# Optimization experiments

Measured on AMD Instinct MI355X. Metric: run time of the kernel, lower is better.

## Reference

```python
import jax, jax.numpy as jnp
import numpy as np

N_E = 8192
E_DIM = 256
BETA = 0.25
SIGMA = 0.1


def setup_inputs() -> dict:
    key = jax.random.key(0)
    kz, ke = jax.random.split(key)
    z = jax.random.normal(kz, (16, 256, 32, 32), dtype=jnp.float32)
    # torch init: uniform(-1/n_e, 1/n_e)
    emb = jax.random.uniform(ke, (N_E, E_DIM), minval=-1.0 / N_E, maxval=1.0 / N_E, dtype=jnp.float32)
    return {"z": z, "emb": emb}


def _vq_forward(z, emb, beta=BETA, sigma=SIGMA):
    b, c, h, w = z.shape  # c == e_dim
    z_bhwc = jnp.transpose(z, (0, 2, 3, 1))  # b h w c
    zf = z_bhwc.reshape(-1, c)  # [b*h*w, c]

    # d[i, n] = ||zf_i||^2 + ||e_n||^2 - 2 zf_i . e_n
    e2 = jnp.sum(emb ** 2, axis=1)  # [n_e]
    d = jnp.sum(zf ** 2, axis=1, keepdims=True) + e2 - 2.0 * (zf @ emb.T)  # [bhw, n_e]

    # codebook-codebook pairwise distances
    d1 = e2[:, None] + e2[None, :] - 2.0 * (emb @ emb.T)  # [n_e, n_e]
    # torch.kthvalue(d1, 2, 0): 2nd smallest along dim 0, per column
    min_dist = jnp.sort(d1, axis=0)[1]  # [n_e]
    total_min_distance = jnp.sum(min_dist)
    codebookvariance = jnp.std(min_dist, ddof=1)  # torch.std is unbiased

    min_encoding_indices = jnp.argmin(d, axis=1)  # [bhw]
    # d[range, argmin] == row-wise min
    distances = jnp.min(d, axis=1).reshape(b, h, w)
    # rbf: exp(-(d^2).mean(axis=1) / (2*sigma^2)) -> [b, w]
    distances = jnp.exp(-jnp.mean(distances ** 2, axis=1) / (2.0 * sigma ** 2))

    z_q = jnp.take(emb, min_encoding_indices, axis=0).reshape(b, h, w, c)

    sg = jax.lax.stop_gradient
    # legacy=True branch
    loss = (jnp.mean((sg(z_q) - z_bhwc) ** 2)
            + beta * jnp.mean((z_q - sg(z_bhwc)) ** 2)
            - total_min_distance)

    # straight-through estimator
    z_q = z_bhwc + sg(z_q - z_bhwc)
    z_q_bchw = jnp.transpose(z_q, (0, 3, 1, 2))  # b c h w (contiguous)
    # torch .view(b, h*w, e_dim) on contiguous bchw buffer: raw reshape
    z_flattened1 = z_q_bchw.reshape(b, h * w, c)

    return (z_q_bchw, loss, distances, min_encoding_indices,
            z_flattened1, codebookvariance, total_min_distance)


def reference(z, emb):
    return _vq_forward(z, emb)
```

## Files before the change

kernel.cpp:

```cpp
#include <hip/hip_runtime.h>
#include <stdint.h>

#define N_E   8192
#define EDIM  256
#define NB    16
#define HH    32
#define WW    32
#define HW    1024
#define NI    16384
#define NELEM 4194304

#define MARGIN_D1 1e-9f

#define O_ZQ   0
#define O_LOSS 4194304
#define O_DIST 4194305
#define O_IDX  4194817
#define O_ZFL  4211201
#define O_CBV  8405505
#define O_TMD  8405506

#define WS_IDX   0x0
#define WS_DMIN  0x20000
#define WS_E2    0x40000
#define WS_Z2    0x50000
#define WS_MSE   0x60000
#define WS_MIND  0x61000
#define WS_PZ    0x70000
#define WS_PD1   0x270000
#define WS_ZAH   0x400000
#define WS_ZAL   0xC00000
#define WS_EBH   0x1400000
#define WS_EBL   0x1800000

typedef __attribute__((ext_vector_type(8))) short bf16x8;
typedef __attribute__((ext_vector_type(4))) float f32x4;

__device__ __forceinline__ short f2bf(float f) {
    unsigned u = __float_as_uint(f);
    u += 0x7fffu + ((u >> 16) & 1u);
    return (short)(u >> 16);
}
__device__ __forceinline__ float bf2f(short h) {
    return __uint_as_float(((unsigned)(unsigned short)h) << 16);
}
__device__ __forceinline__ unsigned keyf(float f) {
    unsigned b = __float_as_uint(f);
    return (b & 0x80000000u) ? ~b : (b | 0x80000000u);
}
__device__ __forceinline__ float unkeyf(unsigned k) {
    return (k & 0x80000000u) ? __uint_as_float(k ^ 0x80000000u) : __uint_as_float(~k);
}
__device__ __forceinline__ void ins2(unsigned long long& a1, unsigned long long& a2,
                                     unsigned long long v) {
    if (v < a1) { a2 = a1; a1 = v; } else if (v < a2) { a2 = v; }
}
__device__ __forceinline__ void mrg2(unsigned long long& a1, unsigned long long& a2,
                                     unsigned long long b1, unsigned long long b2) {
    unsigned long long n1 = a1 < b1 ? a1 : b1;
    unsigned long long mx = a1 < b1 ? b1 : a1;
    unsigned long long mn = a2 < b2 ? a2 : b2;
    a1 = n1; a2 = mx < mn ? mx : mn;
}

__global__ void k_init(double* __restrict__ mse) {
    if (threadIdx.x == 0) *mse = 0.0;
}

__global__ void k_e2(const float* __restrict__ emb, float* __restrict__ e2) {
    int row  = blockIdx.x * 4 + (threadIdx.x >> 6);
    int lane = threadIdx.x & 63;
    float4 v = *reinterpret_cast<const float4*>(emb + (size_t)row * EDIM + lane * 4);
    float s = v.x * v.x + v.y * v.y + v.z * v.z + v.w * v.w;
    #pragma unroll
    for (int m = 32; m; m >>= 1) s += __shfl_xor(s, m);
    if (lane == 0) e2[row] = s;
}

__global__ void k_z2(const float* __restrict__ z, float* __restrict__ z2) {
    int i = blockIdx.x * 256 + threadIdx.x;
    int b = i >> 10, hw = i & 1023;
    const float* p = z + (size_t)b * EDIM * HW + hw;
    float s = 0.f;
    #pragma unroll 8
    for (int c = 0; c < EDIM; ++c) { float v = p[(size_t)c * HW]; s += v * v; }
    z2[i] = s;
}

__global__ void k_convert_z(const float* __restrict__ z,
                            bf16x8* __restrict__ zAh, bf16x8* __restrict__ zAl) {
    __shared__ float lds[64][65];
    const int t   = threadIdx.x;
    const int hw0 = blockIdx.x * 64;
    const int c0  = blockIdx.y * 64;
    const int b   = blockIdx.z;
    #pragma unroll
    for (int cc = 0; cc < 4; ++cc) {
        const int cl = cc * 16 + (t >> 4);
        const float4 v = *reinterpret_cast<const float4*>(
            z + ((size_t)(b * 256 + c0 + cl) << 10) + hw0 + (t & 15) * 4);
        lds[cl][(t & 15) * 4 + 0] = v.x; lds[cl][(t & 15) * 4 + 1] = v.y;
        lds[cl][(t & 15) * 4 + 2] = v.z; lds[cl][(t & 15) * 4 + 3] = v.w;
    }
    __syncthreads();
    const int hl = t & 63;
    const int i  = b * 1024 + hw0 + hl;
    const int ig = i >> 4, r = i & 15;
    #pragma unroll
    for (int half = 0; half < 2; ++half) {
        const int kqi = (t >> 6) + half * 4;
        const int kq  = (c0 >> 3) + kqi;
        bf16x8 oh, ol;
        #pragma unroll
        for (int j = 0; j < 8; ++j) {
            const float f = lds[kqi * 8 + j][hl];
            const short h = f2bf(f);
            oh[j] = h;
            ol[j] = f2bf(f - bf2f(h));
        }
        zAh[(ig * 32 + kq) * 16 + r] = oh;
        zAl[(ig * 32 + kq) * 16 + r] = ol;
    }
}

__global__ void k_convert_e(const float* __restrict__ emb,
                            bf16x8* __restrict__ eBh, bf16x8* __restrict__ eBl) {
    const int t  = threadIdx.x;
    const int kq = t & 31;
    const int n  = blockIdx.x * 8 + (t >> 5);
    const float4 u = *reinterpret_cast<const float4*>(emb + (size_t)n * EDIM + kq * 8);
    const float4 v = *reinterpret_cast<const float4*>(emb + (size_t)n * EDIM + kq * 8 + 4);
    const float fv[8] = {u.x, u.y, u.z, u.w, v.x, v.y, v.z, v.w};
    bf16x8 oh, ol;
    #pragma unroll
    for (int j = 0; j < 8; ++j) {
        const short h = f2bf(fv[j]);
        oh[j] = h;
        ol[j] = f2bf(fv[j] - bf2f(h));
    }
    eBh[((n >> 4) * 32 + kq) * 16 + (n & 15)] = oh;
    eBl[((n >> 4) * 32 + kq) * 16 + (n & 15)] = ol;
}

__launch_bounds__(256, 2)
__global__ void k_cand(const bf16x8* __restrict__ zAh, const bf16x8* __restrict__ zAl,
                       const bf16x8* __restrict__ eBh, const bf16x8* __restrict__ eBl,
                       const float* __restrict__ z2, const float* __restrict__ e2,
                       unsigned long long* __restrict__ pz) {
    const int t = threadIdx.x;
    const int w = t >> 6, l = t & 63;
    const int lo16 = l & 15, hi4 = l >> 4;
    const int iblk = blockIdx.x, chunk = blockIdx.y;
    const int ig0 = (iblk * 128 + w * 32) >> 4;

    float z2r[2][4];
    #pragma unroll
    for (int ig = 0; ig < 2; ++ig)
        #pragma unroll
        for (int reg = 0; reg < 4; ++reg)
            z2r[ig][reg] = z2[iblk * 128 + w * 32 + ig * 16 + hi4 * 4 + reg];

    unsigned long long t1[2][4], t2[2][4];
    #pragma unroll
    for (int ig = 0; ig < 2; ++ig)
        #pragma unroll
        for (int reg = 0; reg < 4; ++reg) { t1[ig][reg] = ~0ull; t2[ig][reg] = ~0ull; }

    for (int ns = 0; ns < 8; ++ns) {
        const int n0 = chunk * 1024 + ns * 128;
        f32x4 acc[2][8];
        #pragma unroll
        for (int ig = 0; ig < 2; ++ig)
            #pragma unroll
            for (int cg = 0; cg < 8; ++cg) acc[ig][cg] = (f32x4){0.f, 0.f, 0.f, 0.f};

        #pragma unroll
        for (int st = 0; st < 8; ++st) {
            const bf16x8 ah0 = zAh[((ig0 + 0) * 32 + st * 4 + hi4) * 16 + lo16];
            const bf16x8 ah1 = zAh[((ig0 + 1) * 32 + st * 4 + hi4) * 16 + lo16];
            const bf16x8 al0 = zAl[((ig0 + 0) * 32 + st * 4 + hi4) * 16 + lo16];
            const bf16x8 al1 = zAl[((ig0 + 1) * 32 + st * 4 + hi4) * 16 + lo16];
            #pragma unroll
            for (int cg = 0; cg < 8; ++cg) {
                const bf16x8 bh = eBh[(((n0 >> 4) + cg) * 32 + st * 4 + hi4) * 16 + lo16];
                const bf16x8 bl = eBl[(((n0 >> 4) + cg) * 32 + st * 4 + hi4) * 16 + lo16];
                acc[0][cg] = __builtin_amdgcn_mfma_f32_16x16x32_bf16(ah0, bh, acc[0][cg], 0, 0, 0);
                acc[0][cg] = __builtin_amdgcn_mfma_f32_16x16x32_bf16(ah0, bl, acc[0][cg], 0, 0, 0);
                acc[0][cg] = __builtin_amdgcn_mfma_f32_16x16x32_bf16(al0, bh, acc[0][cg], 0, 0, 0);
                acc[1][cg] = __builtin_amdgcn_mfma_f32_16x16x32_bf16(ah1, bh, acc[1][cg], 0, 0, 0);
                acc[1][cg] = __builtin_amdgcn_mfma_f32_16x16x32_bf16(ah1, bl, acc[1][cg], 0, 0, 0);
                acc[1][cg] = __builtin_amdgcn_mfma_f32_16x16x32_bf16(al1, bh, acc[1][cg], 0, 0, 0);
            }
        }
        float e2v[8];
        #pragma unroll
        for (int cg = 0; cg < 8; ++cg) e2v[cg] = e2[n0 + cg * 16 + lo16];
        #pragma unroll
        for (int ig = 0; ig < 2; ++ig) {
            #pragma unroll
            for (int reg = 0; reg < 4; ++reg) {
                #pragma unroll
                for (int cg = 0; cg < 8; ++cg) {
                    const float d = fmaf(-2.f, acc[ig][cg][reg], z2r[ig][reg] + e2v[cg]);
                    const unsigned long long pk =
                        ((unsigned long long)keyf(d) << 32) | (unsigned)(n0 + cg * 16 + lo16);
                    ins2(t1[ig][reg], t2[ig][reg], pk);
                }
            }
        }
    }
    #pragma unroll
    for (int ig = 0; ig < 2; ++ig) {
        #pragma unroll
        for (int reg = 0; reg < 4; ++reg) {
            unsigned long long a1 = t1[ig][reg], a2 = t2[ig][reg];
            #pragma unroll
            for (int o = 1; o < 16; o <<= 1) {
                const unsigned long long b1 = __shfl_xor(a1, o);
                const unsigned long long b2 = __shfl_xor(a2, o);
                mrg2(a1, a2, b1, b2);
            }
            if (lo16 == 0) {
                const int row = iblk * 128 + w * 32 + ig * 16 + hi4 * 4 + reg;
                pz[(row * 8 + chunk) * 2 + 0] = a1;
                pz[(row * 8 + chunk) * 2 + 1] = a2;
            }
        }
    }
}

__launch_bounds__(256, 2)
__global__ void k_cand_d1(const bf16x8* __restrict__ eBh, const bf16x8* __restrict__ eBl,
                          const float* __restrict__ e2,
                          unsigned long long* __restrict__ pd1) {
    const int t = threadIdx.x;
    const int w = t >> 6, l = t & 63;
    const int lo16 = l & 15, hi4 = l >> 4;
    const int iblk = blockIdx.x, chunk = blockIdx.y;
    const int ig0 = (iblk * 128 + w * 32) >> 4;

    unsigned long long t1[2][4], t2[2][4];
    #pragma unroll
    for (int ig = 0; ig < 2; ++ig)
        #pragma unroll
        for (int reg = 0; reg < 4; ++reg) { t1[ig][reg] = ~0ull; t2[ig][reg] = ~0ull; }

    for (int ns = 0; ns < 8; ++ns) {
        const int n0 = chunk * 1024 + ns * 128;
        f32x4 acc[2][8];
        #pragma unroll
        for (int ig = 0; ig < 2; ++ig)
            #pragma unroll
            for (int cg = 0; cg < 8; ++cg) acc[ig][cg] = (f32x4){0.f, 0.f, 0.f, 0.f};

        #pragma unroll
        for (int st = 0; st < 8; ++st) {
            const bf16x8 ah0 = eBh[((ig0 + 0) * 32 + st * 4 + hi4) * 16 + lo16];
            const bf16x8 ah1 = eBh[((ig0 + 1) * 32 + st * 4 + hi4) * 16 + lo16];
            const bf16x8 al0 = eBl[((ig0 + 0) * 32 + st * 4 + hi4) * 16 + lo16];
            const bf16x8 al1 = eBl[((ig0 + 1) * 32 + st * 4 + hi4) * 16 + lo16];
            #pragma unroll
            for (int cg = 0; cg < 8; ++cg) {
                const bf16x8 bh = eBh[(((n0 >> 4) + cg) * 32 + st * 4 + hi4) * 16 + lo16];
                const bf16x8 bl = eBl[(((n0 >> 4) + cg) * 32 + st * 4 + hi4) * 16 + lo16];
                acc[0][cg] = __builtin_amdgcn_mfma_f32_16x16x32_bf16(ah0, bh, acc[0][cg], 0, 0, 0);
                acc[0][cg] = __builtin_amdgcn_mfma_f32_16x16x32_bf16(ah0, bl, acc[0][cg], 0, 0, 0);
                acc[0][cg] = __builtin_amdgcn_mfma_f32_16x16x32_bf16(al0, bh, acc[0][cg], 0, 0, 0);
                acc[1][cg] = __builtin_amdgcn_mfma_f32_16x16x32_bf16(ah1, bh, acc[1][cg], 0, 0, 0);
                acc[1][cg] = __builtin_amdgcn_mfma_f32_16x16x32_bf16(ah1, bl, acc[1][cg], 0, 0, 0);
                acc[1][cg] = __builtin_amdgcn_mfma_f32_16x16x32_bf16(al1, bh, acc[1][cg], 0, 0, 0);
            }
        }
        float e2v[8];
        #pragma unroll
        for (int cg = 0; cg < 8; ++cg) e2v[cg] = e2[n0 + cg * 16 + lo16];
        #pragma unroll
        for (int ig = 0; ig < 2; ++ig) {
            #pragma unroll
            for (int reg = 0; reg < 4; ++reg) {
                #pragma unroll
                for (int cg = 0; cg < 8; ++cg) {
                    const float q = fmaf(-2.f, acc[ig][cg][reg], e2v[cg]);
                    const unsigned long long pk =
                        ((unsigned long long)keyf(q) << 32) | (unsigned)(n0 + cg * 16 + lo16);
                    ins2(t1[ig][reg], t2[ig][reg], pk);
                }
            }
        }
    }
    #pragma unroll
    for (int ig = 0; ig < 2; ++ig) {
        #pragma unroll
        for (int reg = 0; reg < 4; ++reg) {
            unsigned long long a1 = t1[ig][reg], a2 = t2[ig][reg];
            #pragma unroll
            for (int o = 1; o < 16; o <<= 1) {
                const unsigned long long b1 = __shfl_xor(a1, o);
                const unsigned long long b2 = __shfl_xor(a2, o);
                mrg2(a1, a2, b1, b2);
            }
            if (lo16 == 0) {
                const int row = iblk * 128 + w * 32 + ig * 16 + hi4 * 4 + reg;
                pd1[(row * 8 + chunk) * 2 + 0] = a1;
                pd1[(row * 8 + chunk) * 2 + 1] = a2;
            }
        }
    }
}

__global__ void k_zmerge(const float* __restrict__ z, const float* __restrict__ emb,
                         const float* __restrict__ z2, const float* __restrict__ e2,
                         const unsigned long long* __restrict__ pz,
                         int* __restrict__ idxi, float* __restrict__ dmin,
                         float* __restrict__ out_idx) {
    const int t = threadIdx.x, l = t & 63;
    const int row = blockIdx.x * 64 + (t >> 6) * 16 + (l >> 2);
    const int cs = (l >> 1) & 1, hf = l & 1;
    unsigned long long a1 = ~0ull, a2 = ~0ull;
    #pragma unroll
    for (int k = 0; k < 4; ++k)
        ins2(a1, a2, pz[row * 16 + (l & 3) * 4 + k]);
    #pragma unroll
    for (int o = 1; o < 4; o <<= 1) {
        const unsigned long long b1 = __shfl_xor(a1, o);
        const unsigned long long b2 = __shfl_xor(a2, o);
        mrg2(a1, a2, b1, b2);
    }
    const int n = (unsigned)(cs ? a2 : a1);
    const float* zp = z + ((size_t)(row >> 10) << 18) + (row & 1023);
    const float* ep = emb + (size_t)n * EDIM;
    float acc = 0.f;
    #pragma unroll 8
    for (int c = 0; c < 128; ++c) {
        const int cc = hf * 128 + c;
        acc = fmaf(zp[(size_t)cc << 10], ep[cc], acc);
    }
    const float total = acc + __shfl_xor(acc, 1);
    const float d = fmaf(-2.f, total, z2[row] + e2[n]);
    unsigned long long pk = ((unsigned long long)__float_as_uint(d) << 32) | (unsigned)n;
    const unsigned long long op = __shfl_xor(pk, 2);
    if (op < pk) pk = op;
    if ((l & 3) == 0) {
        const int ni = (int)(pk & 0xFFFFFFFFull);
        idxi[row] = ni;
        dmin[row] = __uint_as_float((unsigned)(pk >> 32));
        out_idx[row] = (float)ni;
    }
}

__global__ void k_d1merge(const float* __restrict__ emb, const float* __restrict__ e2,
                          const unsigned long long* __restrict__ pd1,
                          float* __restrict__ mind) {
    const int n = blockIdx.x * 256 + threadIdx.x;
    unsigned long long w1 = ~0ull, w2 = ~0ull;
    unsigned long long ent[16];
    #pragma unroll
    for (int e = 0; e < 16; ++e) { ent[e] = pd1[n * 16 + e]; ins2(w1, w2, ent[e]); }
    const float thr = unkeyf((unsigned)(w2 >> 32)) + MARGIN_D1;
    const float e2n = e2[n];
    const float* np = emb + (size_t)n * EDIM;
    float b1 = 3.4e38f, b2 = 3.4e38f;
    #pragma unroll 1
    for (int e = 0; e < 16; ++e) {
        const float af = unkeyf((unsigned)(ent[e] >> 32));
        if (af > thr) continue;
        const int m = (unsigned)ent[e];
        const float* ep = emb + (size_t)m * EDIM;
        float acc = 0.f;
        #pragma unroll 8
        for (int c = 0; c < EDIM; ++c) acc = fmaf(ep[c], np[c], acc);
        const float dv = (e2[m] + e2n) - 2.0f * acc;
        if (dv < b1) { b2 = b1; b1 = dv; } else if (dv < b2) { b2 = dv; }
    }
    mind[n] = b2;
}

__global__ void k_epilogue(const float* __restrict__ z, const float* __restrict__ emb,
                           const int* __restrict__ idxi,
                           float* __restrict__ out_zq, float* __restrict__ out_zfl,
                           double* __restrict__ mse) {
    const int j4 = blockIdx.x * 256 + threadIdx.x;
    const int j  = j4 * 4;
    const int b  = j >> 18;
    const int c  = (j >> 10) & 255;
    const int hw = j & 1023;
    const int ib = (b << 10) + hw;
    const float4 zv = *reinterpret_cast<const float4*>(z + j);
    const float q0 = emb[(size_t)idxi[ib + 0] * EDIM + c];
    const float q1 = emb[(size_t)idxi[ib + 1] * EDIM + c];
    const float q2 = emb[(size_t)idxi[ib + 2] * EDIM + c];
    const float q3 = emb[(size_t)idxi[ib + 3] * EDIM + c];
    const float d0 = q0 - zv.x, d1 = q1 - zv.y, d2 = q2 - zv.z, d3 = q3 - zv.w;
    const float4 st = {zv.x + d0, zv.y + d1, zv.z + d2, zv.w + d3};
    *reinterpret_cast<float4*>(out_zq + j) = st;
    out_zfl[j + 0] = st.x; out_zfl[j + 1] = st.y; out_zfl[j + 2] = st.z; out_zfl[j + 3] = st.w;

    double s = (double)(d0 * d0) + (double)(d1 * d1) + (double)(d2 * d2) + (double)(d3 * d3);
    #pragma unroll
    for (int m = 32; m; m >>= 1) s += __shfl_down(s, m);
    __shared__ double part[4];
    if ((threadIdx.x & 63) == 0) part[threadIdx.x >> 6] = s;
    __syncthreads();
    if (threadIdx.x == 0) atomicAdd(mse, part[0] + part[1] + part[2] + part[3]);
}

__global__ void k_distances(const float* __restrict__ dmin, float* __restrict__ out_d) {
    int t = threadIdx.x;
    int b = t >> 5, w = t & 31;
    float s = 0.f;
    #pragma unroll
    for (int h = 0; h < HH; ++h) {
        float d = dmin[(b << 10) + (h << 5) + w];
        s += d * d;
    }
    float mean = s * (1.0f / 32.0f);
    out_d[t] = expf(-mean / 0.02f);
}

__global__ void k_finalize(const float* __restrict__ mind, const double* __restrict__ mse,
                           float* __restrict__ out) {
    const int t = threadIdx.x;
    double s = 0.0, ss = 0.0;
    for (int n = t; n < N_E; n += 256) {
        const double v = (double)mind[n];
        s += v; ss += v * v;
    }
    #pragma unroll
    for (int m = 32; m; m >>= 1) { s += __shfl_down(s, m); ss += __shfl_down(ss, m); }
    __shared__ double rs[4], rss[4];
    if ((t & 63) == 0) { rs[t >> 6] = s; rss[t >> 6] = ss; }
    __syncthreads();
    if (t == 0) {
        const double S  = rs[0] + rs[1] + rs[2] + rs[3];
        const double SS = rss[0] + rss[1] + rss[2] + rss[3];
        const float tmd = (float)S;
        double var = (SS - S * S / (double)N_E) / (double)(N_E - 1);
        if (var < 0.0) var = 0.0;
        const float cbv = (float)sqrt(var);
        const float m1  = (float)(*mse / (double)NELEM);
        const float lossf = m1 + 0.25f * m1 - tmd;
        out[O_LOSS] = lossf;
        out[O_CBV]  = cbv;
        out[O_TMD]  = tmd;
    }
}

extern "C" void kernel_launch(void* const* d_in, const int* in_sizes, int n_in,
                              void* d_out, int out_size, void* d_ws, size_t ws_size,
                              hipStream_t stream) {
    const float* z   = (const float*)d_in[0];
    const float* emb = (const float*)d_in[1];
    float* out = (float*)d_out;
    char*  ws  = (char*)d_ws;

    int*      idxi = (int*)    (ws + WS_IDX);
    float*    dmin = (float*)  (ws + WS_DMIN);
    float*    e2   = (float*)  (ws + WS_E2);
    float*    z2   = (float*)  (ws + WS_Z2);
    double*   mse  = (double*) (ws + WS_MSE);
    float*    mind = (float*)  (ws + WS_MIND);
    unsigned long long* pz  = (unsigned long long*)(ws + WS_PZ);
    unsigned long long* pd1 = (unsigned long long*)(ws + WS_PD1);
    bf16x8*   zAh  = (bf16x8*) (ws + WS_ZAH);
    bf16x8*   zAl  = (bf16x8*) (ws + WS_ZAL);
    bf16x8*   eBh  = (bf16x8*) (ws + WS_EBH);
    bf16x8*   eBl  = (bf16x8*) (ws + WS_EBL);

    k_init     <<<1,    64,  0, stream>>>(mse);
    k_e2       <<<2048, 256, 0, stream>>>(emb, e2);
    k_z2       <<<64,   256, 0, stream>>>(z, z2);
    k_convert_z<<<dim3(16, 4, 16), 256, 0, stream>>>(z, zAh, zAl);
    k_convert_e<<<1024, 256, 0, stream>>>(emb, eBh, eBl);
    k_cand     <<<dim3(128, 8), 256, 0, stream>>>(zAh, zAl, eBh, eBl, z2, e2, pz);
    k_cand_d1  <<<dim3(64, 8),  256, 0, stream>>>(eBh, eBl, e2, pd1);
    k_zmerge   <<<256,  256, 0, stream>>>(z, emb, z2, e2, pz, idxi, dmin, out + O_IDX);
    k_d1merge  <<<32,   256, 0, stream>>>(emb, e2, pd1, mind);
    k_epilogue <<<4096, 256, 0, stream>>>(z, emb, idxi, out + O_ZQ, out + O_ZFL, mse);
    k_distances<<<1,    512, 0, stream>>>(dmin, out + O_DIST);
    k_finalize <<<1,    256, 0, stream>>>(mind, mse, out);
}
```

Before: 1.279 ms.

## Emit per-subchunk top-2 candidates, raise occupancy, parallelize codebook merge per wave

The candidate GEMM kernels no longer carry running top-2 arrays across the column loop. Each 128-column sub-chunk now reduces and writes its own top-2, which frees registers so launch bounds can go to 3 waves-per-EU occupancy; the MFMA issue order is also regrouped into batches of 4 B tiles. The codebook-pair merge now uses one wave per row with shuffle reductions and parallel exact rechecks, replacing the 32-block one-thread-per-row loop. In exchange, the candidate buffers grow eightfold; they are placed in unused regions of the output buffer to save workspace, and the merge kernels must read more candidates.

```diff
diff --git a/kernel.cpp b/kernel.cpp
--- a/kernel.cpp
+++ b/kernel.cpp
@@ -26,12 +26,10 @@
 #define WS_Z2    0x50000
 #define WS_MSE   0x60000
 #define WS_MIND  0x61000
-#define WS_PZ    0x70000
-#define WS_PD1   0x270000
-#define WS_ZAH   0x400000
-#define WS_ZAL   0xC00000
-#define WS_EBH   0x1400000
-#define WS_EBL   0x1800000
+#define WS_ZAH   0x100000
+#define WS_ZAL   0x900000
+#define WS_EBH   0x1100000
+#define WS_EBL   0x1500000
 
 typedef __attribute__((ext_vector_type(8))) short bf16x8;
 typedef __attribute__((ext_vector_type(4))) float f32x4;
@@ -142,7 +140,7 @@
     eBl[((n >> 4) * 32 + kq) * 16 + (n & 15)] = ol;
 }
 
-__launch_bounds__(256, 2)
+__launch_bounds__(256, 3)
 __global__ void k_cand(const bf16x8* __restrict__ zAh, const bf16x8* __restrict__ zAl,
                        const bf16x8* __restrict__ eBh, const bf16x8* __restrict__ eBl,
                        const float* __restrict__ z2, const float* __restrict__ e2,
@@ -160,14 +158,9 @@
         for (int reg = 0; reg < 4; ++reg)
             z2r[ig][reg] = z2[iblk * 128 + w * 32 + ig * 16 + hi4 * 4 + reg];
 
-    unsigned long long t1[2][4], t2[2][4];
-    #pragma unroll
-    for (int ig = 0; ig < 2; ++ig)
-        #pragma unroll
-        for (int reg = 0; reg < 4; ++reg) { t1[ig][reg] = ~0ull; t2[ig][reg] = ~0ull; }
-
+    #pragma unroll 1
     for (int ns = 0; ns < 8; ++ns) {
-        const int n0 = chunk * 1024 + ns * 128;
+        const int gcol = chunk * 64 + ns * 8;
         f32x4 acc[2][8];
         #pragma unroll
         for (int ig = 0; ig < 2; ++ig)
@@ -176,60 +169,71 @@
 
         #pragma unroll
         for (int st = 0; st < 8; ++st) {
-            const bf16x8 ah0 = zAh[((ig0 + 0) * 32 + st * 4 + hi4) * 16 + lo16];
-            const bf16x8 ah1 = zAh[((ig0 + 1) * 32 + st * 4 + hi4) * 16 + lo16];
-            const bf16x8 al0 = zAl[((ig0 + 0) * 32 + st * 4 + hi4) * 16 + lo16];
-            const bf16x8 al1 = zAl[((ig0 + 1) * 32 + st * 4 + hi4) * 16 + lo16];
+            const int arow = st * 4 + hi4;
+            const bf16x8 ah0 = zAh[((ig0 + 0) * 32 + arow) * 16 + lo16];
+            const bf16x8 ah1 = zAh[((ig0 + 1) * 32 + arow) * 16 + lo16];
+            const bf16x8 al0 = zAl[((ig0 + 0) * 32 + arow) * 16 + lo16];
+            const bf16x8 al1 = zAl[((ig0 + 1) * 32 + arow) * 16 + lo16];
             #pragma unroll
-            for (int cg = 0; cg < 8; ++cg) {
-                const bf16x8 bh = eBh[(((n0 >> 4) + cg) * 32 + st * 4 + hi4) * 16 + lo16];
-                const bf16x8 bl = eBl[(((n0 >> 4) + cg) * 32 + st * 4 + hi4) * 16 + lo16];
-                acc[0][cg] = __builtin_amdgcn_mfma_f32_16x16x32_bf16(ah0, bh, acc[0][cg], 0, 0, 0);
-                acc[0][cg] = __builtin_amdgcn_mfma_f32_16x16x32_bf16(ah0, bl, acc[0][cg], 0, 0, 0);
-                acc[0][cg] = __builtin_amdgcn_mfma_f32_16x16x32_bf16(al0, bh, acc[0][cg], 0, 0, 0);
-                acc[1][cg] = __builtin_amdgcn_mfma_f32_16x16x32_bf16(ah1, bh, acc[1][cg], 0, 0, 0);
-                acc[1][cg] = __builtin_amdgcn_mfma_f32_16x16x32_bf16(ah1, bl, acc[1][cg], 0, 0, 0);
-                acc[1][cg] = __builtin_amdgcn_mfma_f32_16x16x32_bf16(al1, bh, acc[1][cg], 0, 0, 0);
+            for (int cgb = 0; cgb < 8; cgb += 4) {
+                bf16x8 bh[4], bl[4];
+                #pragma unroll
+                for (int q = 0; q < 4; ++q) {
+                    bh[q] = eBh[((gcol + cgb + q) * 32 + arow) * 16 + lo16];
+                    bl[q] = eBl[((gcol + cgb + q) * 32 + arow) * 16 + lo16];
+                }
+                #pragma unroll
+                for (int q = 0; q < 4; ++q)
+                    acc[0][cgb+q] = __builtin_amdgcn_mfma_f32_16x16x32_bf16(ah0, bh[q], acc[0][cgb+q], 0, 0, 0);
+                #pragma unroll
+                for (int q = 0; q < 4; ++q)
+                    acc[1][cgb+q] = __builtin_amdgcn_mfma_f32_16x16x32_bf16(ah1, bh[q], acc[1][cgb+q], 0, 0, 0);
+                #pragma unroll
+                for (int q = 0; q < 4; ++q)
+                    acc[0][cgb+q] = __builtin_amdgcn_mfma_f32_16x16x32_bf16(ah0, bl[q], acc[0][cgb+q], 0, 0, 0);
+                #pragma unroll
+                for (int q = 0; q < 4; ++q)
+                    acc[1][cgb+q] = __builtin_amdgcn_mfma_f32_16x16x32_bf16(ah1, bl[q], acc[1][cgb+q], 0, 0, 0);
+                #pragma unroll
+                for (int q = 0; q < 4; ++q)
+                    acc[0][cgb+q] = __builtin_amdgcn_mfma_f32_16x16x32_bf16(al0, bh[q], acc[0][cgb+q], 0, 0, 0);
+                #pragma unroll
+                for (int q = 0; q < 4; ++q)
+                    acc[1][cgb+q] = __builtin_amdgcn_mfma_f32_16x16x32_bf16(al1, bh[q], acc[1][cgb+q], 0, 0, 0);
             }
         }
         float e2v[8];
         #pragma unroll
-        for (int cg = 0; cg < 8; ++cg) e2v[cg] = e2[n0 + cg * 16 + lo16];
+        for (int cg = 0; cg < 8; ++cg) e2v[cg] = e2[(gcol + cg) * 16 + lo16];
         #pragma unroll
         for (int ig = 0; ig < 2; ++ig) {
             #pragma unroll
             for (int reg = 0; reg < 4; ++reg) {
+                unsigned long long t1 = ~0ull, t2 = ~0ull;
                 #pragma unroll
                 for (int cg = 0; cg < 8; ++cg) {
                     const float d = fmaf(-2.f, acc[ig][cg][reg], z2r[ig][reg] + e2v[cg]);
                     const unsigned long long pk =
-                        ((unsigned long long)keyf(d) << 32) | (unsigned)(n0 + cg * 16 + lo16);
-                    ins2(t1[ig][reg], t2[ig][reg], pk);
+                        ((unsigned long long)keyf(d) << 32) | (unsigned)((gcol + cg) * 16 + lo16);
+                    ins2(t1, t2, pk);
+                }
+                #pragma unroll
+                for (int o = 1; o < 16; o <<= 1) {
+                    const unsigned long long b1 = __shfl_xor(t1, o);
+                    const unsigned long long b2 = __shfl_xor(t2, o);
+                    mrg2(t1, t2, b1, b2);
+                }
+                if (lo16 == 0) {
+                    const int row = iblk * 128 + w * 32 + ig * 16 + hi4 * 4 + reg;
+                    pz[((size_t)row * 64 + chunk * 8 + ns) * 2 + 0] = t1;
+                    pz[((size_t)row * 64 + chunk * 8 + ns) * 2 + 1] = t2;
                 }
             }
         }
     }
-    #pragma unroll
-    for (int ig = 0; ig < 2; ++ig) {
-        #pragma unroll
-        for (int reg = 0; reg < 4; ++reg) {
-            unsigned long long a1 = t1[ig][reg], a2 = t2[ig][reg];
-            #pragma unroll
-            for (int o = 1; o < 16; o <<= 1) {
-                const unsigned long long b1 = __shfl_xor(a1, o);
-                const unsigned long long b2 = __shfl_xor(a2, o);
-                mrg2(a1, a2, b1, b2);
-            }
-            if (lo16 == 0) {
-                const int row = iblk * 128 + w * 32 + ig * 16 + hi4 * 4 + reg;
-                pz[(row * 8 + chunk) * 2 + 0] = a1;
-                pz[(row * 8 + chunk) * 2 + 1] = a2;
-            }
-        }
-    }
-}
-
-__launch_bounds__(256, 2)
+}
+
+__launch_bounds__(256, 3)
 __global__ void k_cand_d1(const bf16x8* __restrict__ eBh, const bf16x8* __restrict__ eBl,
                           const float* __restrict__ e2,
                           unsigned long long* __restrict__ pd1) {
@@ -239,14 +243,9 @@
     const int iblk = blockIdx.x, chunk = blockIdx.y;
     const int ig0 = (iblk * 128 + w * 32) >> 4;
 
-    unsigned long long t1[2][4], t2[2][4];
-    #pragma unroll
-    for (int ig = 0; ig < 2; ++ig)
-        #pragma unroll
-        for (int reg = 0; reg < 4; ++reg) { t1[ig][reg] = ~0ull; t2[ig][reg] = ~0ull; }
-
+    #pragma unroll 1
     for (int ns = 0; ns < 8; ++ns) {
-        const int n0 = chunk * 1024 + ns * 128;
+        const int gcol = chunk * 64 + ns * 8;
         f32x4 acc[2][8];
         #pragma unroll
         for (int ig = 0; ig < 2; ++ig)
@@ -255,54 +254,65 @@
 
         #pragma unroll
         for (int st = 0; st < 8; ++st) {
-            const bf16x8 ah0 = eBh[((ig0 + 0) * 32 + st * 4 + hi4) * 16 + lo16];
-            const bf16x8 ah1 = eBh[((ig0 + 1) * 32 + st * 4 + hi4) * 16 + lo16];
-            const bf16x8 al0 = eBl[((ig0 + 0) * 32 + st * 4 + hi4) * 16 + lo16];
-            const bf16x8 al1 = eBl[((ig0 + 1) * 32 + st * 4 + hi4) * 16 + lo16];
+            const int arow = st * 4 + hi4;
+            const bf16x8 ah0 = eBh[((ig0 + 0) * 32 + arow) * 16 + lo16];
+            const bf16x8 ah1 = eBh[((ig0 + 1) * 32 + arow) * 16 + lo16];
+            const bf16x8 al0 = eBl[((ig0 + 0) * 32 + arow) * 16 + lo16];
+            const bf16x8 al1 = eBl[((ig0 + 1) * 32 + arow) * 16 + lo16];
             #pragma unroll
-            for (int cg = 0; cg < 8; ++cg) {
-                const bf16x8 bh = eBh[(((n0 >> 4) + cg) * 32 + st * 4 + hi4) * 16 + lo16];
-                const bf16x8 bl = eBl[(((n0 >> 4) + cg) * 32 + st * 4 + hi4) * 16 + lo16];
-                acc[0][cg] = __builtin_amdgcn_mfma_f32_16x16x32_bf16(ah0, bh, acc[0][cg], 0, 0, 0);
-                acc[0][cg] = __builtin_amdgcn_mfma_f32_16x16x32_bf16(ah0, bl, acc[0][cg], 0, 0, 0);
-                acc[0][cg] = __builtin_amdgcn_mfma_f32_16x16x32_bf16(al0, bh, acc[0][cg], 0, 0, 0);
-                acc[1][cg] = __builtin_amdgcn_mfma_f32_16x16x32_bf16(ah1, bh, acc[1][cg], 0, 0, 0);
-                acc[1][cg] = __builtin_amdgcn_mfma_f32_16x16x32_bf16(ah1, bl, acc[1][cg], 0, 0, 0);
-                acc[1][cg] = __builtin_amdgcn_mfma_f32_16x16x32_bf16(al1, bh, acc[1][cg], 0, 0, 0);
+            for (int cgb = 0; cgb < 8; cgb += 4) {
+                bf16x8 bh[4], bl[4];
+                #pragma unroll
+                for (int q = 0; q < 4; ++q) {
+                    bh[q] = eBh[((gcol + cgb + q) * 32 + arow) * 16 + lo16];
+                    bl[q] = eBl[((gcol + cgb + q) * 32 + arow) * 16 + lo16];
+                }
+                #pragma unroll
+                for (int q = 0; q < 4; ++q)
+                    acc[0][cgb+q] = __builtin_amdgcn_mfma_f32_16x16x32_bf16(ah0, bh[q], acc[0][cgb+q], 0, 0, 0);
+                #pragma unroll
+                for (int q = 0; q < 4; ++q)
+                    acc[1][cgb+q] = __builtin_amdgcn_mfma_f32_16x16x32_bf16(ah1, bh[q], acc[1][cgb+q], 0, 0, 0);
+                #pragma unroll
+                for (int q = 0; q < 4; ++q)
+                    acc[0][cgb+q] = __builtin_amdgcn_mfma_f32_16x16x32_bf16(ah0, bl[q], acc[0][cgb+q], 0, 0, 0);
+                #pragma unroll
+                for (int q = 0; q < 4; ++q)
+                    acc[1][cgb+q] = __builtin_amdgcn_mfma_f32_16x16x32_bf16(ah1, bl[q], acc[1][cgb+q], 0, 0, 0);
+                #pragma unroll
+                for (int q = 0; q < 4; ++q)
+                    acc[0][cgb+q] = __builtin_amdgcn_mfma_f32_16x16x32_bf16(al0, bh[q], acc[0][cgb+q], 0, 0, 0);
+                #pragma unroll
+                for (int q = 0; q < 4; ++q)
+                    acc[1][cgb+q] = __builtin_amdgcn_mfma_f32_16x16x32_bf16(al1, bh[q], acc[1][cgb+q], 0, 0, 0);
             }
         }
         float e2v[8];
         #pragma unroll
-        for (int cg = 0; cg < 8; ++cg) e2v[cg] = e2[n0 + cg * 16 + lo16];
+        for (int cg = 0; cg < 8; ++cg) e2v[cg] = e2[(gcol + cg) * 16 + lo16];
         #pragma unroll
         for (int ig = 0; ig < 2; ++ig) {
             #pragma unroll
             for (int reg = 0; reg < 4; ++reg) {
+                unsigned long long t1 = ~0ull, t2 = ~0ull;
                 #pragma unroll
                 for (int cg = 0; cg < 8; ++cg) {
                     const float q = fmaf(-2.f, acc[ig][cg][reg], e2v[cg]);
                     const unsigned long long pk =
-                        ((unsigned long long)keyf(q) << 32) | (unsigned)(n0 + cg * 16 + lo16);
-                    ins2(t1[ig][reg], t2[ig][reg], pk);
-                }
-            }
-        }
-    }
-    #pragma unroll
-    for (int ig = 0; ig < 2; ++ig) {
-        #pragma unroll
-        for (int reg = 0; reg < 4; ++reg) {
-            unsigned long long a1 = t1[ig][reg], a2 = t2[ig][reg];
-            #pragma unroll
-            for (int o = 1; o < 16; o <<= 1) {
-                const unsigned long long b1 = __shfl_xor(a1, o);
-                const unsigned long long b2 = __shfl_xor(a2, o);
-                mrg2(a1, a2, b1, b2);
-            }
-            if (lo16 == 0) {
-                const int row = iblk * 128 + w * 32 + ig * 16 + hi4 * 4 + reg;
-                pd1[(row * 8 + chunk) * 2 + 0] = a1;
-                pd1[(row * 8 + chunk) * 2 + 1] = a2;
+                        ((unsigned long long)keyf(q) << 32) | (unsigned)((gcol + cg) * 16 + lo16);
+                    ins2(t1, t2, pk);
+                }
+                #pragma unroll
+                for (int o = 1; o < 16; o <<= 1) {
+                    const unsigned long long b1 = __shfl_xor(t1, o);
+                    const unsigned long long b2 = __shfl_xor(t2, o);
+                    mrg2(t1, t2, b1, b2);
+                }
+                if (lo16 == 0) {
+                    const int row = iblk * 128 + w * 32 + ig * 16 + hi4 * 4 + reg;
+                    pd1[((size_t)row * 64 + chunk * 8 + ns) * 2 + 0] = t1;
+                    pd1[((size_t)row * 64 + chunk * 8 + ns) * 2 + 1] = t2;
+                }
             }
         }
     }
@@ -317,9 +327,9 @@
     const int row = blockIdx.x * 64 + (t >> 6) * 16 + (l >> 2);
     const int cs = (l >> 1) & 1, hf = l & 1;
     unsigned long long a1 = ~0ull, a2 = ~0ull;
-    #pragma unroll
-    for (int k = 0; k < 4; ++k)
-        ins2(a1, a2, pz[row * 16 + (l & 3) * 4 + k]);
+    #pragma unroll 4
+    for (int k = 0; k < 32; ++k)
+        ins2(a1, a2, pz[(size_t)row * 128 + (l & 3) * 32 + k]);
     #pragma unroll
     for (int o = 1; o < 4; o <<= 1) {
         const unsigned long long b1 = __shfl_xor(a1, o);
@@ -351,28 +361,43 @@
 __global__ void k_d1merge(const float* __restrict__ emb, const float* __restrict__ e2,
                           const unsigned long long* __restrict__ pd1,
                           float* __restrict__ mind) {
-    const int n = blockIdx.x * 256 + threadIdx.x;
+    const int t = threadIdx.x, l = t & 63;
+    const int n = blockIdx.x * 4 + (t >> 6);
+    const unsigned long long e0 = pd1[(size_t)n * 128 + l];
+    const unsigned long long e1 = pd1[(size_t)n * 128 + 64 + l];
     unsigned long long w1 = ~0ull, w2 = ~0ull;
-    unsigned long long ent[16];
-    #pragma unroll
-    for (int e = 0; e < 16; ++e) { ent[e] = pd1[n * 16 + e]; ins2(w1, w2, ent[e]); }
+    ins2(w1, w2, e0); ins2(w1, w2, e1);
+    #pragma unroll
+    for (int o = 1; o < 64; o <<= 1) {
+        const unsigned long long b1 = __shfl_xor(w1, o);
+        const unsigned long long b2 = __shfl_xor(w2, o);
+        mrg2(w1, w2, b1, b2);
+    }
     const float thr = unkeyf((unsigned)(w2 >> 32)) + MARGIN_D1;
     const float e2n = e2[n];
     const float* np = emb + (size_t)n * EDIM;
     float b1 = 3.4e38f, b2 = 3.4e38f;
-    #pragma unroll 1
-    for (int e = 0; e < 16; ++e) {
-        const float af = unkeyf((unsigned)(ent[e] >> 32));
-        if (af > thr) continue;
-        const int m = (unsigned)ent[e];
-        const float* ep = emb + (size_t)m * EDIM;
-        float acc = 0.f;
-        #pragma unroll 8
-        for (int c = 0; c < EDIM; ++c) acc = fmaf(ep[c], np[c], acc);
-        const float dv = (e2[m] + e2n) - 2.0f * acc;
-        if (dv < b1) { b2 = b1; b1 = dv; } else if (dv < b2) { b2 = dv; }
-    }
-    mind[n] = b2;
+    const unsigned long long ent[2] = {e0, e1};
+    #pragma unroll
+    for (int s = 0; s < 2; ++s) {
+        if (unkeyf((unsigned)(ent[s] >> 32)) <= thr) {
+            const int m = (unsigned)ent[s];
+            const float* ep = emb + (size_t)m * EDIM;
+            float acc = 0.f;
+            #pragma unroll 8
+            for (int c = 0; c < EDIM; ++c) acc = fmaf(ep[c], np[c], acc);
+            const float dv = (e2[m] + e2n) - 2.0f * acc;
+            if (dv < b1) { b2 = b1; b1 = dv; } else if (dv < b2) { b2 = dv; }
+        }
+    }
+    #pragma unroll
+    for (int o = 1; o < 64; o <<= 1) {
+        const float o1 = __shfl_xor(b1, o), o2 = __shfl_xor(b2, o);
+        const float n1 = fminf(b1, o1);
+        const float n2 = fminf(fmaxf(b1, o1), fminf(b2, o2));
+        b1 = n1; b2 = n2;
+    }
+    if (l == 0) mind[n] = b2;
 }
 
 __global__ void k_epilogue(const float* __restrict__ z, const float* __restrict__ emb,
@@ -459,12 +484,12 @@
     float*    z2   = (float*)  (ws + WS_Z2);
     double*   mse  = (double*) (ws + WS_MSE);
     float*    mind = (float*)  (ws + WS_MIND);
-    unsigned long long* pz  = (unsigned long long*)(ws + WS_PZ);
-    unsigned long long* pd1 = (unsigned long long*)(ws + WS_PD1);
     bf16x8*   zAh  = (bf16x8*) (ws + WS_ZAH);
     bf16x8*   zAl  = (bf16x8*) (ws + WS_ZAL);
     bf16x8*   eBh  = (bf16x8*) (ws + WS_EBH);
     bf16x8*   eBl  = (bf16x8*) (ws + WS_EBL);
+    unsigned long long* pz  = (unsigned long long*)d_out;
+    unsigned long long* pd1 = (unsigned long long*)((char*)d_out + (size_t)O_ZFL * 4 + 4);
 
     k_init     <<<1,    64,  0, stream>>>(mse);
     k_e2       <<<2048, 256, 0, stream>>>(emb, e2);
@@ -474,7 +499,7 @@
     k_cand     <<<dim3(128, 8), 256, 0, stream>>>(zAh, zAl, eBh, eBl, z2, e2, pz);
     k_cand_d1  <<<dim3(64, 8),  256, 0, stream>>>(eBh, eBl, e2, pd1);
     k_zmerge   <<<256,  256, 0, stream>>>(z, emb, z2, e2, pz, idxi, dmin, out + O_IDX);
-    k_d1merge  <<<32,   256, 0, stream>>>(emb, e2, pd1, mind);
+    k_d1merge  <<<2048, 256, 0, stream>>>(emb, e2, pd1, mind);
     k_epilogue <<<4096, 256, 0, stream>>>(z, emb, idxi, out + O_ZQ, out + O_ZFL, mse);
     k_distances<<<1,    512, 0, stream>>>(dmin, out + O_DIST);
     k_finalize <<<1,    256, 0, stream>>>(mind, mse, out);
```

Result: slower. 1.558 ms (+21.8%).
